# Optimization experiments

Hardware: AMD Instinct MI355X
Metric: run time of the kernel (lower is better)

Reference implementation:

```python
import math
import jax
import jax.numpy as jnp
import numpy as np

H = 16
D_MODEL = 1024
D_K = D_MODEL // H            # 64
POS_DK = D_MODEL // 4 // H    # 16
EMB_DIM = D_MODEL // 4        # 256
MAX_DIST = 1000
RES = 20                      # RealEmbedding discretization resolution (3rd ctor arg)
N_EMB = 2 * MAX_DIST * RES + 1
B, NQ, NK = 2, 512, 512


def setup_inputs() -> dict:
    key0 = jax.random.key(0)
    ks = jax.random.split(key0, 16)
    s = 0.02

    def lin(k, din, dout):
        return (jax.random.normal(k, (din, dout), jnp.float32) * s,
                jnp.zeros((dout,), jnp.float32))

    Wq, bq = lin(ks[7], D_MODEL, D_MODEL)
    Wk, bk = lin(ks[8], D_MODEL, D_MODEL)
    Wv, bv = lin(ks[9], D_MODEL, D_MODEL)
    Wo, bo = lin(ks[10], D_MODEL, D_MODEL)
    Wb, bb = lin(ks[11], POS_DK, 1)
    return {
        "query": jax.random.normal(ks[0], (B, NQ, D_MODEL), jnp.float32),
        "key": jax.random.normal(ks[1], (B, NK, D_MODEL), jnp.float32),
        "value": jax.random.normal(ks[2], (B, NK, D_MODEL), jnp.float32),
        "query_x": jax.random.uniform(ks[3], (B, NQ), jnp.float32, 0.0, float(MAX_DIST)),
        "query_y": jax.random.uniform(ks[4], (B, NQ), jnp.float32, 0.0, float(MAX_DIST)),
        "key_x": jax.random.uniform(ks[5], (B, NK), jnp.float32, 0.0, float(MAX_DIST)),
        "key_y": jax.random.uniform(ks[6], (B, NK), jnp.float32, 0.0, float(MAX_DIST)),
        "Wq": Wq, "bq": bq, "Wk": Wk, "bk": bk, "Wv": Wv, "bv": bv,
        "Wo": Wo, "bo": bo,
        "x_table": jax.random.normal(ks[12], (N_EMB, EMB_DIM), jnp.float32) * s,
        "y_table": jax.random.normal(ks[13], (N_EMB, EMB_DIM), jnp.float32) * s,
        "Wb": Wb, "bb": bb,
    }


def _real_emb(table, d):
    # RealEmbedding: clamp real-valued distance to [-MAX_DIST, MAX_DIST],
    # discretize at resolution RES, nearest-neighbor table lookup.
    idx = jnp.round((jnp.clip(d, -MAX_DIST, MAX_DIST) + MAX_DIST) * RES).astype(jnp.int32)
    return table[idx]


def _forward(query, key, value, query_x, query_y, key_x, key_y,
             Wq, bq, Wk, bk, Wv, bv, Wo, bo, x_table, y_table, Wb, bb):
    b, nq, _ = query.shape
    nk = key.shape[1]
    # relative-position differences, layout (b, nk, nq) exactly as the torch expand
    x_diff = query_x[:, None, :] - key_x[:, :, None]
    y_diff = query_y[:, None, :] - key_y[:, :, None]
    pos_emb = _real_emb(x_table, x_diff) + _real_emb(y_table, y_diff)  # (b, nk, nq, EMB_DIM)
    pos_emb = pos_emb.reshape(b, nk, nq, H, POS_DK)
    att_bias = jax.nn.sigmoid((pos_emb @ Wb + bb)[..., 0])  # (b, nk, nq, H)
    # permute(0,3,1,2): (b, H, nk, nq); added to (b, H, nq, nk) scores (self-attn, nq==nk)
    att_bias = att_bias.transpose(0, 3, 1, 2)
    q = (query @ Wq + bq).reshape(b, nq, H, D_K).transpose(0, 2, 1, 3)
    k = (key @ Wk + bk).reshape(b, nk, H, D_K).transpose(0, 2, 1, 3)
    v = (value @ Wv + bv).reshape(b, nk, H, D_K).transpose(0, 2, 1, 3)
    scores = jnp.einsum('bhqd,bhkd->bhqk', q, k) / math.sqrt(D_K) + att_bias
    p_attn = jax.nn.softmax(scores, axis=-1)  # dropout p=0 / eval mode
    out = jnp.einsum('bhqk,bhkd->bhqd', p_attn, v)
    out = out.transpose(0, 2, 1, 3).reshape(b, nq, D_MODEL)
    return out @ Wo + bo


def reference(query, key, value, query_x, query_y, key_x, key_y,
              Wq, bq, Wk, bk, Wv, bv, Wo, bo, x_table, y_table, Wb, bb):
    return _forward(query, key, value, query_x, query_y, key_x, key_y,
                    Wq, bq, Wk, bk, Wv, bv, Wo, bo, x_table, y_table, Wb, bb)
```

## Files before the change

### kernel.cpp

```cpp
#include <hip/hip_runtime.h>
#include <math.h>

#define HH 16
#define DM 1024
#define DK 64
#define NE 40001
#define NB 2
#define NQS 512
#define NKS 512

typedef unsigned short ushort_t;
typedef __attribute__((ext_vector_type(8))) short short8v;
typedef __attribute__((ext_vector_type(4))) float f32x4;

__device__ __forceinline__ ushort_t f2bf(float f) {
    union { float f; unsigned u; } v; v.f = f;
    unsigned r = v.u + 0x7FFFu + ((v.u >> 16) & 1u);
    return (ushort_t)(r >> 16);
}
__device__ __forceinline__ unsigned pack2(float a, float b) {
    return (unsigned)f2bf(a) | ((unsigned)f2bf(b) << 16);
}
__device__ __forceinline__ float asf(unsigned u) {
    union { unsigned u; float f; } v; v.u = u; return v.f;
}

#define PROJ_F4   (NE * 64)
#define PROJ_TOT  (2 * PROJ_F4)
#define PREP_PROJ_BLKS 1024
#define PREP_WT_BLKS   512
#define PREP_QKV_BLKS  256

__global__ __launch_bounds__(256) void prep_k(
    const float* __restrict__ xt, const float* __restrict__ yt,
    const float* __restrict__ Wb,
    const float* __restrict__ wq, const float* __restrict__ wk,
    const float* __restrict__ wv, const float* __restrict__ wo,
    const float* __restrict__ xq, const float* __restrict__ xk, const float* __restrict__ xv,
    ushort_t* __restrict__ xproj, ushort_t* __restrict__ yproj,
    ushort_t* __restrict__ wqt, ushort_t* __restrict__ wkt,
    ushort_t* __restrict__ wvt, ushort_t* __restrict__ wot,
    ushort_t* __restrict__ qc, ushort_t* __restrict__ kc, ushort_t* __restrict__ vc)
{
    __shared__ float ls[64][68];
    const int bid = blockIdx.x;
    const int tid = threadIdx.x;

    if (bid < PREP_PROJ_BLKS) {
        const int c = tid & 3;
        const float4 wq4 = ((const float4*)Wb)[c];
#pragma unroll 4
        for (int f4 = bid * 256 + tid; f4 < PROJ_TOT; f4 += PREP_PROJ_BLKS * 256) {
            const int tsel = (f4 >= PROJ_F4);
            const int g = tsel ? f4 - PROJ_F4 : f4;
            const float* tab = tsel ? yt : xt;
            float4 v = ((const float4*)tab)[g];
            float p = v.x * wq4.x + v.y * wq4.y + v.z * wq4.z + v.w * wq4.w;
            p += __shfl_xor(p, 1);
            p += __shfl_xor(p, 2);
            if (c == 0) {
                ushort_t* dst = tsel ? yproj : xproj;
                const int i = g >> 6, h = (g >> 2) & 15;
                dst[i * 16 + h] = f2bf(p);
            }
        }
    } else if (bid < PREP_PROJ_BLKS + PREP_WT_BLKS) {
        const int b0 = bid - PREP_PROJ_BLKS;
#pragma unroll
        for (int it = 0; it < 2; ++it) {
            const int t = b0 + it * PREP_WT_BLKS;
            const int z = t >> 8;
            const int rem = t & 255;
            const int k0 = (rem >> 4) * 64, n0 = (rem & 15) * 64;
            const float* w = (z == 0) ? wq : ((z == 1) ? wk : ((z == 2) ? wv : wo));
            ushort_t* wt = (z == 0) ? wqt : ((z == 1) ? wkt : ((z == 2) ? wvt : wot));

            if (it) __syncthreads();
#pragma unroll
            for (int j = 0; j < 4; ++j) {
                int r = (tid >> 4) + j * 16;
                int c2 = (tid & 15) * 4;
                float4 v = *(const float4*)(w + (k0 + r) * 1024 + n0 + c2);
                *(float4*)&ls[r][c2] = v;
            }
            __syncthreads();

            const int n = tid >> 2, kq = (tid & 3) * 16;
            float e[16];
#pragma unroll
            for (int j = 0; j < 16; ++j) e[j] = ls[kq + j][n];
            uint4 o0, o1;
            o0.x = pack2(e[0], e[1]);   o0.y = pack2(e[2], e[3]);
            o0.z = pack2(e[4], e[5]);   o0.w = pack2(e[6], e[7]);
            o1.x = pack2(e[8], e[9]);   o1.y = pack2(e[10], e[11]);
            o1.z = pack2(e[12], e[13]); o1.w = pack2(e[14], e[15]);
            ushort_t* dp = wt + (n0 + n) * 1024 + k0 + kq;
            *(uint4*)(dp)     = o0;
            *(uint4*)(dp + 8) = o1;
        }
    } else {
        const int b0 = bid - (PREP_PROJ_BLKS + PREP_WT_BLKS);
#pragma unroll 4
        for (int f4 = b0 * 256 + tid; f4 < 786432; f4 += PREP_QKV_BLKS * 256) {
            const int z = f4 >> 18;
            const int g = f4 & 262143;
            const float* src = (z == 0) ? xq : ((z == 1) ? xk : xv);
            ushort_t* dst = (z == 0) ? qc : ((z == 1) ? kc : vc);
            float4 a = ((const float4*)src)[g];
            uint2 o;
            o.x = pack2(a.x, a.y); o.y = pack2(a.z, a.w);
            *reinterpret_cast<uint2*>(dst + g * 4) = o;
        }
    }
}

__global__ __launch_bounds__(256, 6) void biasqkv_k(
    const ushort_t* __restrict__ A0, const ushort_t* __restrict__ A1, const ushort_t* __restrict__ A2,
    const ushort_t* __restrict__ B0, const ushort_t* __restrict__ B1, const ushort_t* __restrict__ B2,
    const float* __restrict__ bi0, const float* __restrict__ bi1, const float* __restrict__ bi2,
    ushort_t* __restrict__ Yh0, ushort_t* __restrict__ Yh1, ushort_t* __restrict__ Yh2,
    const ushort_t* __restrict__ xproj, const ushort_t* __restrict__ yproj,
    const float* __restrict__ qx, const float* __restrict__ qy,
    const float* __restrict__ kx, const float* __restrict__ ky,
    const float* __restrict__ bbp,
    ushort_t* __restrict__ biasf)
{
    __shared__ ushort_t As[64][72];
    __shared__ ushort_t Bs[64][72];
    const int bid = blockIdx.x;
    const int tid = threadIdx.x;

    if (bid < 768) {
        const int z = bid >> 8, by = (bid >> 4) & 15, bx = bid & 15;
        const ushort_t* Ah = (z == 0) ? A0 : ((z == 1) ? A1 : A2);
        const ushort_t* Bp = (z == 0) ? B0 : ((z == 1) ? B1 : B2);
        const float* bi = (z == 0) ? bi0 : ((z == 1) ? bi1 : bi2);
        ushort_t* Yh = (z == 0) ? Yh0 : ((z == 1) ? Yh1 : Yh2);
        const int m0 = by * 64, n0 = bx * 64;
        const int lane = tid & 63, w = tid >> 6;
        const int wm = w >> 1, wn = w & 1;
        const int srow = tid >> 2, scg = (tid & 3) * 16;

        f32x4 acc[2][2] = {};
        uint4 arh0, arh1, brh0, brh1;

        auto loadA = [&](int kk) {
            const ushort_t* ap = Ah + (m0 + srow) * 1024 + kk + scg;
            arh0 = *(const uint4*)(ap);
            arh1 = *(const uint4*)(ap + 8);
        };
        auto loadB = [&](int kk) {
            const ushort_t* bp = Bp + (n0 + srow) * 1024 + kk + scg;
            brh0 = *(const uint4*)(bp);
            brh1 = *(const uint4*)(bp + 8);
        };
        loadA(0); loadB(0);

        const int fr = lane & 15;
        const int ko = (lane >> 4) * 8;

        for (int k0 = 0; k0 < 1024; k0 += 64) {
            __syncthreads();
            *(uint4*)&As[srow][scg]     = arh0;
            *(uint4*)&As[srow][scg + 8] = arh1;
            *(uint4*)&Bs[srow][scg]     = brh0;
            *(uint4*)&Bs[srow][scg + 8] = brh1;
            __syncthreads();
            if (k0 + 64 < 1024) { loadA(k0 + 64); loadB(k0 + 64); }
#pragma unroll
            for (int ks = 0; ks < 64; ks += 32) {
                short8v af0 = *(const short8v*)&As[wm * 32 + fr][ks + ko];
                short8v af1 = *(const short8v*)&As[wm * 32 + 16 + fr][ks + ko];
                short8v bf0 = *(const short8v*)&Bs[wn * 32 + fr][ks + ko];
                short8v bf1 = *(const short8v*)&Bs[wn * 32 + 16 + fr][ks + ko];
                acc[0][0] = __builtin_amdgcn_mfma_f32_16x16x32_bf16(af0, bf0, acc[0][0], 0, 0, 0);
                acc[0][1] = __builtin_amdgcn_mfma_f32_16x16x32_bf16(af0, bf1, acc[0][1], 0, 0, 0);
                acc[1][0] = __builtin_amdgcn_mfma_f32_16x16x32_bf16(af1, bf0, acc[1][0], 0, 0, 0);
                acc[1][1] = __builtin_amdgcn_mfma_f32_16x16x32_bf16(af1, bf1, acc[1][1], 0, 0, 0);
            }
        }

        const int cr = (lane >> 4) * 4;
        const int cc = lane & 15;
#pragma unroll
        for (int m = 0; m < 2; ++m) {
#pragma unroll
            for (int n = 0; n < 2; ++n) {
                int grow = m0 + wm * 32 + m * 16 + cr;
                int gcol = n0 + wn * 32 + n * 16 + cc;
                float bv = bi[gcol];
                int hh = gcol >> 6, dd = gcol & 63;
                if (z == 0) {
#pragma unroll
                    for (int j = 0; j < 4; ++j) {
                        int r = grow + j, bb_ = r >> 9, nn = r & 511;
                        Yh[((bb_ * HH + hh) * NQS + nn) * DK + dd] = f2bf(acc[m][n][j] + bv);
                    }
                } else if (z == 1) {
#pragma unroll
                    for (int j = 0; j < 4; ++j) {
                        int r = grow + j, bb_ = r >> 9, nn = r & 511;
                        Yh[((bb_ * HH + hh) * NQS + nn) * DK + dd] = f2bf((acc[m][n][j] + bv) * 0.125f);
                    }
                } else {
#pragma unroll
                    for (int j = 0; j < 4; ++j) {
                        int r = grow + j, bb_ = r >> 9, nn = r & 511;
                        Yh[((bb_ * HH + hh) * DK + dd) * NKS + nn] = f2bf(acc[m][n][j] + bv);
                    }
                }
            }
        }
    } else {
        const int r = bid - 768;
        const int b = r >> 10;
        const int kt = (r >> 5) & 31, qt = r & 31;
        const int ql = tid & 15, kl = tid >> 4;
        const int qg = qt * 16 + ql, kg = kt * 16 + kl;

        float dx = qx[b * NKS + kg] - kx[b * NQS + qg];
        float dy = qy[b * NKS + kg] - ky[b * NQS + qg];
        int ix = (int)rintf((fminf(fmaxf(dx, -1000.f), 1000.f) + 1000.f) * 20.f);
        int iy = (int)rintf((fminf(fmaxf(dy, -1000.f), 1000.f) + 1000.f) * 20.f);
        const float bb = bbp[0];

        uint4 xw0 = *(const uint4*)(xproj + ix * 16);
        uint4 xw1 = *(const uint4*)(xproj + ix * 16 + 8);
        uint4 yw0 = *(const uint4*)(yproj + iy * 16);
        uint4 yw1 = *(const uint4*)(yproj + iy * 16 + 8);

        float xa[16], ya[16];
        {
            unsigned u[8] = {xw0.x, xw0.y, xw0.z, xw0.w, xw1.x, xw1.y, xw1.z, xw1.w};
            unsigned v[8] = {yw0.x, yw0.y, yw0.z, yw0.w, yw1.x, yw1.y, yw1.z, yw1.w};
#pragma unroll
            for (int wv = 0; wv < 8; ++wv) {
                xa[2 * wv]     = asf(u[wv] << 16);
                xa[2 * wv + 1] = asf(u[wv] & 0xFFFF0000u);
                ya[2 * wv]     = asf(v[wv] << 16);
                ya[2 * wv + 1] = asf(v[wv] & 0xFFFF0000u);
            }
        }
        const int lane_j = ((kl >> 2) * 16 + ql) * 4 + (kl & 3);
#pragma unroll
        for (int h = 0; h < HH; ++h) {
            float t2 = xa[h] + ya[h] + bb;
            float sig = 1.f / (1.f + __expf(-t2));
            biasf[((b * HH + h) * 32 + kt) * (32 * 256) + qt * 256 + lane_j] = f2bf(sig);
        }
    }
}

__global__ __launch_bounds__(256, 4) void attn_k(
    const ushort_t* __restrict__ qbh, const ushort_t* __restrict__ kbh,
    const ushort_t* __restrict__ vtb, const ushort_t* __restrict__ biasf,
    ushort_t* __restrict__ attb)
{
    __shared__ ushort_t pst[4][16][40];
    __shared__ float obuf[4][16][76];
    __shared__ float mt[4][16], lt[4][16];

    const int tid = threadIdx.x;
    const int wid = tid >> 6, lane = tid & 63;
    const int q = lane & 15, g = lane >> 4;
    const int qt = blockIdx.x;
    const int h = blockIdx.y, b = blockIdx.z;
    const int bh = b * HH + h;

    const ushort_t* Qp = qbh + (bh * NQS + qt * 16 + q) * DK + g * 8;
    short8v qf0 = *(const short8v*)Qp;
    short8v qf1 = *(const short8v*)(Qp + 32);

    f32x4 oacc[4] = {};
    float m = -1e30f, l = 0.f;

#pragma unroll 2
    for (int c = 0; c < 4; ++c) {
        const int kc = wid * 128 + c * 32;
        const ushort_t* Kp = kbh + (bh * NKS + kc + q) * DK + g * 8;
        short8v kf00 = *(const short8v*)(Kp);
        short8v kf01 = *(const short8v*)(Kp + 32);
        short8v kf10 = *(const short8v*)(Kp + 16 * DK);
        short8v kf11 = *(const short8v*)(Kp + 16 * DK + 32);

        f32x4 s0 = {0.f, 0.f, 0.f, 0.f};
        f32x4 s1 = {0.f, 0.f, 0.f, 0.f};
        s0 = __builtin_amdgcn_mfma_f32_16x16x32_bf16(kf00, qf0, s0, 0, 0, 0);
        s0 = __builtin_amdgcn_mfma_f32_16x16x32_bf16(kf01, qf1, s0, 0, 0, 0);
        s1 = __builtin_amdgcn_mfma_f32_16x16x32_bf16(kf10, qf0, s1, 0, 0, 0);
        s1 = __builtin_amdgcn_mfma_f32_16x16x32_bf16(kf11, qf1, s1, 0, 0, 0);

        const int kt = kc >> 4;
        uint2 b0 = *((const uint2*)(biasf + ((bh * 32 + kt) * 32 + qt) * 256) + lane);
        uint2 b1 = *((const uint2*)(biasf + ((bh * 32 + kt + 1) * 32 + qt) * 256) + lane);

        float sv[8];
        sv[0] = s0[0] + asf(b0.x << 16);
        sv[1] = s0[1] + asf(b0.x & 0xFFFF0000u);
        sv[2] = s0[2] + asf(b0.y << 16);
        sv[3] = s0[3] + asf(b0.y & 0xFFFF0000u);
        sv[4] = s1[0] + asf(b1.x << 16);
        sv[5] = s1[1] + asf(b1.x & 0xFFFF0000u);
        sv[6] = s1[2] + asf(b1.y << 16);
        sv[7] = s1[3] + asf(b1.y & 0xFFFF0000u);

        float mc = fmaxf(fmaxf(fmaxf(sv[0], sv[1]), fmaxf(sv[2], sv[3])),
                         fmaxf(fmaxf(sv[4], sv[5]), fmaxf(sv[6], sv[7])));
        mc = fmaxf(mc, __shfl_xor(mc, 16));
        mc = fmaxf(mc, __shfl_xor(mc, 32));
        float mn = fmaxf(m, mc);

        float p[8], ps = 0.f;
#pragma unroll
        for (int j = 0; j < 8; ++j) { p[j] = __expf(sv[j] - mn); ps += p[j]; }
        float sc = __expf(m - mn);
        l = l * sc + ps;
        m = mn;
#pragma unroll
        for (int dt = 0; dt < 4; ++dt)
#pragma unroll
            for (int j = 0; j < 4; ++j) oacc[dt][j] *= sc;

        ushort_t* prow = &pst[wid][q][0];
        *(unsigned*)(prow + 4 * g)          = pack2(p[0], p[1]);
        *(unsigned*)(prow + 4 * g + 2)      = pack2(p[2], p[3]);
        *(unsigned*)(prow + 16 + 4 * g)     = pack2(p[4], p[5]);
        *(unsigned*)(prow + 16 + 4 * g + 2) = pack2(p[6], p[7]);
        short8v pf = *(const short8v*)&pst[wid][q][8 * g];

        const ushort_t* Vp = vtb + (bh * DK + q) * NKS + kc + g * 8;
#pragma unroll
        for (int dt = 0; dt < 4; ++dt) {
            short8v vf = *(const short8v*)(Vp + dt * 16 * NKS);
            oacc[dt] = __builtin_amdgcn_mfma_f32_16x16x32_bf16(vf, pf, oacc[dt], 0, 0, 0);
        }
    }

    float lr = l + __shfl_xor(l, 16);
    lr = lr + __shfl_xor(lr, 32);
    if (lane < 16) { mt[wid][lane] = m; lt[wid][lane] = lr; }
#pragma unroll
    for (int dt = 0; dt < 4; ++dt)
#pragma unroll
        for (int j = 0; j < 4; ++j)
            obuf[wid][q][dt * 16 + 4 * g + j] = oacc[dt][j];
    __syncthreads();

    const int mq = tid >> 4, d4 = (tid & 15) * 4;
    float m0 = mt[0][mq], m1 = mt[1][mq], m2 = mt[2][mq], m3 = mt[3][mq];
    float ms = fmaxf(fmaxf(m0, m1), fmaxf(m2, m3));
    float e0 = __expf(m0 - ms), e1 = __expf(m1 - ms);
    float e2 = __expf(m2 - ms), e3 = __expf(m3 - ms);
    float denom = lt[0][mq] * e0 + lt[1][mq] * e1 + lt[2][mq] * e2 + lt[3][mq] * e3;
    float inv = 1.f / denom;
    float4 o0 = *(float4*)&obuf[0][mq][d4];
    float4 o1 = *(float4*)&obuf[1][mq][d4];
    float4 o2 = *(float4*)&obuf[2][mq][d4];
    float4 o3 = *(float4*)&obuf[3][mq][d4];
    float r0 = (o0.x * e0 + o1.x * e1 + o2.x * e2 + o3.x * e3) * inv;
    float r1 = (o0.y * e0 + o1.y * e1 + o2.y * e2 + o3.y * e3) * inv;
    float r2 = (o0.z * e0 + o1.z * e1 + o2.z * e2 + o3.z * e3) * inv;
    float r3 = (o0.w * e0 + o1.w * e1 + o2.w * e2 + o3.w * e3) * inv;
    uint2 ow;
    ow.x = pack2(r0, r1); ow.y = pack2(r2, r3);
    *reinterpret_cast<uint2*>(attb + (b * NQS + qt * 16 + mq) * DM + h * DK + d4) = ow;
}

__global__ __launch_bounds__(256) void ogemm_k(
    const ushort_t* __restrict__ Ah, const ushort_t* __restrict__ Bp,
    const float* __restrict__ bi, float* __restrict__ Yf)
{
    __shared__ ushort_t As[64][72];
    __shared__ ushort_t Bs[64][72];
    const int m0 = blockIdx.y * 64, n0 = blockIdx.x * 64;
    const int tid = threadIdx.x;
    const int lane = tid & 63, w = tid >> 6;
    const int wm = w >> 1, wn = w & 1;
    const int srow = tid >> 2, scg = (tid & 3) * 16;

    f32x4 acc[2][2] = {};
    uint4 arh0, arh1, brh0, brh1;

    auto loadA = [&](int kk) {
        const ushort_t* ap = Ah + (m0 + srow) * 1024 + kk + scg;
        arh0 = *(const uint4*)(ap);
        arh1 = *(const uint4*)(ap + 8);
    };
    auto loadB = [&](int kk) {
        const ushort_t* bp = Bp + (n0 + srow) * 1024 + kk + scg;
        brh0 = *(const uint4*)(bp);
        brh1 = *(const uint4*)(bp + 8);
    };
    loadA(0); loadB(0);

    const int fr = lane & 15;
    const int ko = (lane >> 4) * 8;

    for (int k0 = 0; k0 < 1024; k0 += 64) {
        __syncthreads();
        *(uint4*)&As[srow][scg]     = arh0;
        *(uint4*)&As[srow][scg + 8] = arh1;
        *(uint4*)&Bs[srow][scg]     = brh0;
        *(uint4*)&Bs[srow][scg + 8] = brh1;
        __syncthreads();
        if (k0 + 64 < 1024) { loadA(k0 + 64); loadB(k0 + 64); }
#pragma unroll
        for (int ks = 0; ks < 64; ks += 32) {
            short8v af0 = *(const short8v*)&As[wm * 32 + fr][ks + ko];
            short8v af1 = *(const short8v*)&As[wm * 32 + 16 + fr][ks + ko];
            short8v bf0 = *(const short8v*)&Bs[wn * 32 + fr][ks + ko];
            short8v bf1 = *(const short8v*)&Bs[wn * 32 + 16 + fr][ks + ko];
            acc[0][0] = __builtin_amdgcn_mfma_f32_16x16x32_bf16(af0, bf0, acc[0][0], 0, 0, 0);
            acc[0][1] = __builtin_amdgcn_mfma_f32_16x16x32_bf16(af0, bf1, acc[0][1], 0, 0, 0);
            acc[1][0] = __builtin_amdgcn_mfma_f32_16x16x32_bf16(af1, bf0, acc[1][0], 0, 0, 0);
            acc[1][1] = __builtin_amdgcn_mfma_f32_16x16x32_bf16(af1, bf1, acc[1][1], 0, 0, 0);
        }
    }

    const int cr = (lane >> 4) * 4;
    const int cc = lane & 15;
#pragma unroll
    for (int m = 0; m < 2; ++m) {
#pragma unroll
        for (int n = 0; n < 2; ++n) {
            int grow = m0 + wm * 32 + m * 16 + cr;
            int gcol = n0 + wn * 32 + n * 16 + cc;
            float bv = bi[gcol];
#pragma unroll
            for (int j = 0; j < 4; ++j)
                Yf[(grow + j) * 1024 + gcol] = acc[m][n][j] + bv;
        }
    }
}

extern "C" void kernel_launch(void* const* d_in, const int* in_sizes, int n_in,
                              void* d_out, int out_size, void* d_ws, size_t ws_size,
                              hipStream_t stream)
{
    const float* query = (const float*)d_in[0];
    const float* key   = (const float*)d_in[1];
    const float* value = (const float*)d_in[2];
    const float* qx    = (const float*)d_in[3];
    const float* qy    = (const float*)d_in[4];
    const float* kx    = (const float*)d_in[5];
    const float* ky    = (const float*)d_in[6];
    const float* Wq    = (const float*)d_in[7];
    const float* bq    = (const float*)d_in[8];
    const float* Wk    = (const float*)d_in[9];
    const float* bk    = (const float*)d_in[10];
    const float* Wv    = (const float*)d_in[11];
    const float* bv    = (const float*)d_in[12];
    const float* Wo    = (const float*)d_in[13];
    const float* bo    = (const float*)d_in[14];
    const float* xt    = (const float*)d_in[15];
    const float* yt    = (const float*)d_in[16];
    const float* Wb    = (const float*)d_in[17];
    const float* bbp   = (const float*)d_in[18];
    float* out = (float*)d_out;

    ushort_t* xprojh = (ushort_t*)d_ws;
    ushort_t* yprojh = xprojh + 640064;
    ushort_t* biasf  = yprojh + 640064;
    ushort_t* qbh    = biasf + 8388608;
    ushort_t* kbh    = qbh + 1048576;
    ushort_t* vtb    = kbh + 1048576;
    ushort_t* attb   = vtb + 1048576;
    ushort_t* wqt    = attb + 1048576;
    ushort_t* wkt    = wqt + 1048576;
    ushort_t* wvt    = wkt + 1048576;
    ushort_t* wot    = wvt + 1048576;
    ushort_t* qc     = wot + 1048576;
    ushort_t* kc     = qc + 1048576;
    ushort_t* vc     = kc + 1048576;

    prep_k<<<dim3(PREP_PROJ_BLKS + PREP_WT_BLKS + PREP_QKV_BLKS), dim3(256), 0, stream>>>(
        xt, yt, Wb, Wq, Wk, Wv, Wo, query, key, value,
        xprojh, yprojh, wqt, wkt, wvt, wot, qc, kc, vc);
    biasqkv_k<<<dim3(768 + 2048), dim3(256), 0, stream>>>(
        qc, kc, vc, wqt, wkt, wvt, bq, bk, bv, qbh, kbh, vtb,
        xprojh, yprojh, qx, qy, kx, ky, bbp, biasf);
    attn_k<<<dim3(32, 16, 2), dim3(256), 0, stream>>>(
        qbh, kbh, vtb, biasf, attb);
    ogemm_k<<<dim3(16, 16), dim3(256), 0, stream>>>(
        attb, wot, bo, out);
}
```

Before: 78.33 us.

## Fuse fp32-to-bf16 conversion into QKV GEMM and overlap with table projection

The separate prep pass that converted query/key/value and Wq/Wk/Wv to bf16 (and transposed the weights) is removed. The QKV projection GEMM now reads fp32 activations and weights directly, converting and transposing in registers before writing to shared memory. That GEMM is interleaved in one launch with the table-projection and Wo-transpose blocks, so the work that reads the embedding tables overlaps with the matrix multiply. The bias computation becomes its own kernel. This cuts a global round trip of bf16 intermediates, but the GEMM now issues fp32 loads and scattered 2-byte shared-memory stores for B, which may cause bank conflicts and extra per-iteration conversion work.

```diff
diff --git a/kernel.cpp b/kernel.cpp
--- a/kernel.cpp
+++ b/kernel.cpp
@@ -27,30 +27,33 @@
 
 #define PROJ_F4   (NE * 64)
 #define PROJ_TOT  (2 * PROJ_F4)
-#define PREP_PROJ_BLKS 1024
-#define PREP_WT_BLKS   512
-#define PREP_QKV_BLKS  256
-
-__global__ __launch_bounds__(256) void prep_k(
+#define K1_BLKS   2048
+
+__global__ __launch_bounds__(256, 4) void fused1_k(
     const float* __restrict__ xt, const float* __restrict__ yt,
     const float* __restrict__ Wb,
     const float* __restrict__ wq, const float* __restrict__ wk,
     const float* __restrict__ wv, const float* __restrict__ wo,
-    const float* __restrict__ xq, const float* __restrict__ xk, const float* __restrict__ xv,
+    const float* __restrict__ query, const float* __restrict__ key, const float* __restrict__ value,
+    const float* __restrict__ bq, const float* __restrict__ bk, const float* __restrict__ bv,
     ushort_t* __restrict__ xproj, ushort_t* __restrict__ yproj,
-    ushort_t* __restrict__ wqt, ushort_t* __restrict__ wkt,
-    ushort_t* __restrict__ wvt, ushort_t* __restrict__ wot,
-    ushort_t* __restrict__ qc, ushort_t* __restrict__ kc, ushort_t* __restrict__ vc)
+    ushort_t* __restrict__ wot,
+    ushort_t* __restrict__ qbh, ushort_t* __restrict__ kbh, ushort_t* __restrict__ vtb)
 {
-    __shared__ float ls[64][68];
+    __shared__ __align__(16) unsigned char smem[18944];
+    ushort_t (*As)[72] = (ushort_t(*)[72])smem;
+    ushort_t (*Bs)[72] = (ushort_t(*)[72])(smem + 9472);
+    float (*ls)[68] = (float(*)[68])smem;
+
     const int bid = blockIdx.x;
     const int tid = threadIdx.x;
 
-    if (bid < PREP_PROJ_BLKS) {
+    if (!(bid & 1)) {
+        const int pb = bid >> 1;
         const int c = tid & 3;
         const float4 wq4 = ((const float4*)Wb)[c];
 #pragma unroll 4
-        for (int f4 = bid * 256 + tid; f4 < PROJ_TOT; f4 += PREP_PROJ_BLKS * 256) {
+        for (int f4 = pb * 256 + tid; f4 < PROJ_TOT; f4 += 1024 * 256) {
             const int tsel = (f4 >= PROJ_F4);
             const int g = tsel ? f4 - PROJ_F4 : f4;
             const float* tab = tsel ? yt : xt;
@@ -64,190 +67,181 @@
                 dst[i * 16 + h] = f2bf(p);
             }
         }
-    } else if (bid < PREP_PROJ_BLKS + PREP_WT_BLKS) {
-        const int b0 = bid - PREP_PROJ_BLKS;
-#pragma unroll
-        for (int it = 0; it < 2; ++it) {
-            const int t = b0 + it * PREP_WT_BLKS;
-            const int z = t >> 8;
-            const int rem = t & 255;
-            const int k0 = (rem >> 4) * 64, n0 = (rem & 15) * 64;
-            const float* w = (z == 0) ? wq : ((z == 1) ? wk : ((z == 2) ? wv : wo));
-            ushort_t* wt = (z == 0) ? wqt : ((z == 1) ? wkt : ((z == 2) ? wvt : wot));
-
-            if (it) __syncthreads();
-#pragma unroll
-            for (int j = 0; j < 4; ++j) {
-                int r = (tid >> 4) + j * 16;
-                int c2 = (tid & 15) * 4;
-                float4 v = *(const float4*)(w + (k0 + r) * 1024 + n0 + c2);
-                *(float4*)&ls[r][c2] = v;
+        return;
+    }
+
+    const int u = bid >> 1;
+    if (u >= 768) {
+        const int rem = u - 768;
+        const int k0 = (rem >> 4) * 64, n0 = (rem & 15) * 64;
+#pragma unroll
+        for (int j = 0; j < 4; ++j) {
+            int r = (tid >> 4) + j * 16;
+            int c2 = (tid & 15) * 4;
+            float4 v = *(const float4*)(wo + (k0 + r) * 1024 + n0 + c2);
+            *(float4*)&ls[r][c2] = v;
+        }
+        __syncthreads();
+        const int n = tid >> 2, kq = (tid & 3) * 16;
+        float e[16];
+#pragma unroll
+        for (int j = 0; j < 16; ++j) e[j] = ls[kq + j][n];
+        uint4 o0, o1;
+        o0.x = pack2(e[0], e[1]);   o0.y = pack2(e[2], e[3]);
+        o0.z = pack2(e[4], e[5]);   o0.w = pack2(e[6], e[7]);
+        o1.x = pack2(e[8], e[9]);   o1.y = pack2(e[10], e[11]);
+        o1.z = pack2(e[12], e[13]); o1.w = pack2(e[14], e[15]);
+        ushort_t* dp = wot + (n0 + n) * 1024 + k0 + kq;
+        *(uint4*)(dp)     = o0;
+        *(uint4*)(dp + 8) = o1;
+        return;
+    }
+
+    const int z = u >> 8, by = (u >> 4) & 15, bx = u & 15;
+    const float* Af = (z == 0) ? query : ((z == 1) ? key : value);
+    const float* Wf = (z == 0) ? wq : ((z == 1) ? wk : wv);
+    const float* bi = (z == 0) ? bq : ((z == 1) ? bk : bv);
+    ushort_t* Yh = (z == 0) ? qbh : ((z == 1) ? kbh : vtb);
+    const int m0 = by * 64, n0 = bx * 64;
+    const int lane = tid & 63, w = tid >> 6;
+    const int wm = w >> 1, wn = w & 1;
+    const int srow = tid >> 2, scg = (tid & 3) * 16;
+    const int br_ = tid >> 4, bc = (tid & 15) * 4;
+
+    f32x4 acc[2][2] = {};
+    float4 arf0, arf1, arf2, arf3;
+    float4 brf0, brf1, brf2, brf3;
+
+    auto loadA = [&](int kk) {
+        const float* ap = Af + (m0 + srow) * 1024 + kk + scg;
+        arf0 = *(const float4*)(ap);
+        arf1 = *(const float4*)(ap + 4);
+        arf2 = *(const float4*)(ap + 8);
+        arf3 = *(const float4*)(ap + 12);
+    };
+    auto loadB = [&](int kk) {
+        brf0 = *(const float4*)(Wf + (kk + br_)      * 1024 + n0 + bc);
+        brf1 = *(const float4*)(Wf + (kk + br_ + 16) * 1024 + n0 + bc);
+        brf2 = *(const float4*)(Wf + (kk + br_ + 32) * 1024 + n0 + bc);
+        brf3 = *(const float4*)(Wf + (kk + br_ + 48) * 1024 + n0 + bc);
+    };
+    loadA(0); loadB(0);
+
+    const int fr = lane & 15;
+    const int ko = (lane >> 4) * 8;
+
+    for (int k0 = 0; k0 < 1024; k0 += 64) {
+        __syncthreads();
+        {
+            uint4 w0, w1;
+            w0.x = pack2(arf0.x, arf0.y); w0.y = pack2(arf0.z, arf0.w);
+            w0.z = pack2(arf1.x, arf1.y); w0.w = pack2(arf1.z, arf1.w);
+            w1.x = pack2(arf2.x, arf2.y); w1.y = pack2(arf2.z, arf2.w);
+            w1.z = pack2(arf3.x, arf3.y); w1.w = pack2(arf3.z, arf3.w);
+            *(uint4*)&As[srow][scg]     = w0;
+            *(uint4*)&As[srow][scg + 8] = w1;
+        }
+        {
+            Bs[bc + 0][br_] = f2bf(brf0.x); Bs[bc + 1][br_] = f2bf(brf0.y);
+            Bs[bc + 2][br_] = f2bf(brf0.z); Bs[bc + 3][br_] = f2bf(brf0.w);
+            Bs[bc + 0][br_ + 16] = f2bf(brf1.x); Bs[bc + 1][br_ + 16] = f2bf(brf1.y);
+            Bs[bc + 2][br_ + 16] = f2bf(brf1.z); Bs[bc + 3][br_ + 16] = f2bf(brf1.w);
+            Bs[bc + 0][br_ + 32] = f2bf(brf2.x); Bs[bc + 1][br_ + 32] = f2bf(brf2.y);
+            Bs[bc + 2][br_ + 32] = f2bf(brf2.z); Bs[bc + 3][br_ + 32] = f2bf(brf2.w);
+            Bs[bc + 0][br_ + 48] = f2bf(brf3.x); Bs[bc + 1][br_ + 48] = f2bf(brf3.y);
+            Bs[bc + 2][br_ + 48] = f2bf(brf3.z); Bs[bc + 3][br_ + 48] = f2bf(brf3.w);
+        }
+        __syncthreads();
+        if (k0 + 64 < 1024) { loadA(k0 + 64); loadB(k0 + 64); }
+#pragma unroll
+        for (int ks = 0; ks < 64; ks += 32) {
+            short8v af0 = *(const short8v*)&As[wm * 32 + fr][ks + ko];
+            short8v af1 = *(const short8v*)&As[wm * 32 + 16 + fr][ks + ko];
+            short8v bf0 = *(const short8v*)&Bs[wn * 32 + fr][ks + ko];
+            short8v bf1 = *(const short8v*)&Bs[wn * 32 + 16 + fr][ks + ko];
+            acc[0][0] = __builtin_amdgcn_mfma_f32_16x16x32_bf16(af0, bf0, acc[0][0], 0, 0, 0);
+            acc[0][1] = __builtin_amdgcn_mfma_f32_16x16x32_bf16(af0, bf1, acc[0][1], 0, 0, 0);
+            acc[1][0] = __builtin_amdgcn_mfma_f32_16x16x32_bf16(af1, bf0, acc[1][0], 0, 0, 0);
+            acc[1][1] = __builtin_amdgcn_mfma_f32_16x16x32_bf16(af1, bf1, acc[1][1], 0, 0, 0);
+        }
+    }
+
+    const int cr = (lane >> 4) * 4;
+    const int cc = lane & 15;
+#pragma unroll
+    for (int m = 0; m < 2; ++m) {
+#pragma unroll
+        for (int n = 0; n < 2; ++n) {
+            int grow = m0 + wm * 32 + m * 16 + cr;
+            int gcol = n0 + wn * 32 + n * 16 + cc;
+            float bv = bi[gcol];
+            int hh = gcol >> 6, dd = gcol & 63;
+            if (z == 0) {
+#pragma unroll
+                for (int j = 0; j < 4; ++j) {
+                    int r = grow + j, bb_ = r >> 9, nn = r & 511;
+                    Yh[((bb_ * HH + hh) * NQS + nn) * DK + dd] = f2bf(acc[m][n][j] + bv);
+                }
+            } else if (z == 1) {
+#pragma unroll
+                for (int j = 0; j < 4; ++j) {
+                    int r = grow + j, bb_ = r >> 9, nn = r & 511;
+                    Yh[((bb_ * HH + hh) * NQS + nn) * DK + dd] = f2bf((acc[m][n][j] + bv) * 0.125f);
+                }
+            } else {
+#pragma unroll
+                for (int j = 0; j < 4; ++j) {
+                    int r = grow + j, bb_ = r >> 9, nn = r & 511;
+                    Yh[((bb_ * HH + hh) * DK + dd) * NKS + nn] = f2bf(acc[m][n][j] + bv);
+                }
             }
-            __syncthreads();
-
-            const int n = tid >> 2, kq = (tid & 3) * 16;
-            float e[16];
-#pragma unroll
-            for (int j = 0; j < 16; ++j) e[j] = ls[kq + j][n];
-            uint4 o0, o1;
-            o0.x = pack2(e[0], e[1]);   o0.y = pack2(e[2], e[3]);
-            o0.z = pack2(e[4], e[5]);   o0.w = pack2(e[6], e[7]);
-            o1.x = pack2(e[8], e[9]);   o1.y = pack2(e[10], e[11]);
-            o1.z = pack2(e[12], e[13]); o1.w = pack2(e[14], e[15]);
-            ushort_t* dp = wt + (n0 + n) * 1024 + k0 + kq;
-            *(uint4*)(dp)     = o0;
-            *(uint4*)(dp + 8) = o1;
-        }
-    } else {
-        const int b0 = bid - (PREP_PROJ_BLKS + PREP_WT_BLKS);
-#pragma unroll 4
-        for (int f4 = b0 * 256 + tid; f4 < 786432; f4 += PREP_QKV_BLKS * 256) {
-            const int z = f4 >> 18;
-            const int g = f4 & 262143;
-            const float* src = (z == 0) ? xq : ((z == 1) ? xk : xv);
-            ushort_t* dst = (z == 0) ? qc : ((z == 1) ? kc : vc);
-            float4 a = ((const float4*)src)[g];
-            uint2 o;
-            o.x = pack2(a.x, a.y); o.y = pack2(a.z, a.w);
-            *reinterpret_cast<uint2*>(dst + g * 4) = o;
-        }
-    }
-}
-
-__global__ __launch_bounds__(256, 6) void biasqkv_k(
-    const ushort_t* __restrict__ A0, const ushort_t* __restrict__ A1, const ushort_t* __restrict__ A2,
-    const ushort_t* __restrict__ B0, const ushort_t* __restrict__ B1, const ushort_t* __restrict__ B2,
-    const float* __restrict__ bi0, const float* __restrict__ bi1, const float* __restrict__ bi2,
-    ushort_t* __restrict__ Yh0, ushort_t* __restrict__ Yh1, ushort_t* __restrict__ Yh2,
+        }
+    }
+}
+
+__global__ __launch_bounds__(256) void bias_k(
     const ushort_t* __restrict__ xproj, const ushort_t* __restrict__ yproj,
     const float* __restrict__ qx, const float* __restrict__ qy,
     const float* __restrict__ kx, const float* __restrict__ ky,
     const float* __restrict__ bbp,
     ushort_t* __restrict__ biasf)
 {
-    __shared__ ushort_t As[64][72];
-    __shared__ ushort_t Bs[64][72];
-    const int bid = blockIdx.x;
     const int tid = threadIdx.x;
-
-    if (bid < 768) {
-        const int z = bid >> 8, by = (bid >> 4) & 15, bx = bid & 15;
-        const ushort_t* Ah = (z == 0) ? A0 : ((z == 1) ? A1 : A2);
-        const ushort_t* Bp = (z == 0) ? B0 : ((z == 1) ? B1 : B2);
-        const float* bi = (z == 0) ? bi0 : ((z == 1) ? bi1 : bi2);
-        ushort_t* Yh = (z == 0) ? Yh0 : ((z == 1) ? Yh1 : Yh2);
-        const int m0 = by * 64, n0 = bx * 64;
-        const int lane = tid & 63, w = tid >> 6;
-        const int wm = w >> 1, wn = w & 1;
-        const int srow = tid >> 2, scg = (tid & 3) * 16;
-
-        f32x4 acc[2][2] = {};
-        uint4 arh0, arh1, brh0, brh1;
-
-        auto loadA = [&](int kk) {
-            const ushort_t* ap = Ah + (m0 + srow) * 1024 + kk + scg;
-            arh0 = *(const uint4*)(ap);
-            arh1 = *(const uint4*)(ap + 8);
-        };
-        auto loadB = [&](int kk) {
-            const ushort_t* bp = Bp + (n0 + srow) * 1024 + kk + scg;
-            brh0 = *(const uint4*)(bp);
-            brh1 = *(const uint4*)(bp + 8);
-        };
-        loadA(0); loadB(0);
-
-        const int fr = lane & 15;
-        const int ko = (lane >> 4) * 8;
-
-        for (int k0 = 0; k0 < 1024; k0 += 64) {
-            __syncthreads();
-            *(uint4*)&As[srow][scg]     = arh0;
-            *(uint4*)&As[srow][scg + 8] = arh1;
-            *(uint4*)&Bs[srow][scg]     = brh0;
-            *(uint4*)&Bs[srow][scg + 8] = brh1;
-            __syncthreads();
-            if (k0 + 64 < 1024) { loadA(k0 + 64); loadB(k0 + 64); }
-#pragma unroll
-            for (int ks = 0; ks < 64; ks += 32) {
-                short8v af0 = *(const short8v*)&As[wm * 32 + fr][ks + ko];
-                short8v af1 = *(const short8v*)&As[wm * 32 + 16 + fr][ks + ko];
-                short8v bf0 = *(const short8v*)&Bs[wn * 32 + fr][ks + ko];
-                short8v bf1 = *(const short8v*)&Bs[wn * 32 + 16 + fr][ks + ko];
-                acc[0][0] = __builtin_amdgcn_mfma_f32_16x16x32_bf16(af0, bf0, acc[0][0], 0, 0, 0);
-                acc[0][1] = __builtin_amdgcn_mfma_f32_16x16x32_bf16(af0, bf1, acc[0][1], 0, 0, 0);
-                acc[1][0] = __builtin_amdgcn_mfma_f32_16x16x32_bf16(af1, bf0, acc[1][0], 0, 0, 0);
-                acc[1][1] = __builtin_amdgcn_mfma_f32_16x16x32_bf16(af1, bf1, acc[1][1], 0, 0, 0);
-            }
-        }
-
-        const int cr = (lane >> 4) * 4;
-        const int cc = lane & 15;
-#pragma unroll
-        for (int m = 0; m < 2; ++m) {
-#pragma unroll
-            for (int n = 0; n < 2; ++n) {
-                int grow = m0 + wm * 32 + m * 16 + cr;
-                int gcol = n0 + wn * 32 + n * 16 + cc;
-                float bv = bi[gcol];
-                int hh = gcol >> 6, dd = gcol & 63;
-                if (z == 0) {
-#pragma unroll
-                    for (int j = 0; j < 4; ++j) {
-                        int r = grow + j, bb_ = r >> 9, nn = r & 511;
-                        Yh[((bb_ * HH + hh) * NQS + nn) * DK + dd] = f2bf(acc[m][n][j] + bv);
-                    }
-                } else if (z == 1) {
-#pragma unroll
-                    for (int j = 0; j < 4; ++j) {
-                        int r = grow + j, bb_ = r >> 9, nn = r & 511;
-                        Yh[((bb_ * HH + hh) * NQS + nn) * DK + dd] = f2bf((acc[m][n][j] + bv) * 0.125f);
-                    }
-                } else {
-#pragma unroll
-                    for (int j = 0; j < 4; ++j) {
-                        int r = grow + j, bb_ = r >> 9, nn = r & 511;
-                        Yh[((bb_ * HH + hh) * DK + dd) * NKS + nn] = f2bf(acc[m][n][j] + bv);
-                    }
-                }
-            }
-        }
-    } else {
-        const int r = bid - 768;
-        const int b = r >> 10;
-        const int kt = (r >> 5) & 31, qt = r & 31;
-        const int ql = tid & 15, kl = tid >> 4;
-        const int qg = qt * 16 + ql, kg = kt * 16 + kl;
-
-        float dx = qx[b * NKS + kg] - kx[b * NQS + qg];
-        float dy = qy[b * NKS + kg] - ky[b * NQS + qg];
-        int ix = (int)rintf((fminf(fmaxf(dx, -1000.f), 1000.f) + 1000.f) * 20.f);
-        int iy = (int)rintf((fminf(fmaxf(dy, -1000.f), 1000.f) + 1000.f) * 20.f);
-        const float bb = bbp[0];
-
-        uint4 xw0 = *(const uint4*)(xproj + ix * 16);
-        uint4 xw1 = *(const uint4*)(xproj + ix * 16 + 8);
-        uint4 yw0 = *(const uint4*)(yproj + iy * 16);
-        uint4 yw1 = *(const uint4*)(yproj + iy * 16 + 8);
-
-        float xa[16], ya[16];
-        {
-            unsigned u[8] = {xw0.x, xw0.y, xw0.z, xw0.w, xw1.x, xw1.y, xw1.z, xw1.w};
-            unsigned v[8] = {yw0.x, yw0.y, yw0.z, yw0.w, yw1.x, yw1.y, yw1.z, yw1.w};
-#pragma unroll
-            for (int wv = 0; wv < 8; ++wv) {
-                xa[2 * wv]     = asf(u[wv] << 16);
-                xa[2 * wv + 1] = asf(u[wv] & 0xFFFF0000u);
-                ya[2 * wv]     = asf(v[wv] << 16);
-                ya[2 * wv + 1] = asf(v[wv] & 0xFFFF0000u);
-            }
-        }
-        const int lane_j = ((kl >> 2) * 16 + ql) * 4 + (kl & 3);
-#pragma unroll
-        for (int h = 0; h < HH; ++h) {
-            float t2 = xa[h] + ya[h] + bb;
-            float sig = 1.f / (1.f + __expf(-t2));
-            biasf[((b * HH + h) * 32 + kt) * (32 * 256) + qt * 256 + lane_j] = f2bf(sig);
-        }
+    const int r = blockIdx.x;
+    const int b = r >> 10;
+    const int kt = (r >> 5) & 31, qt = r & 31;
+    const int ql = tid & 15, kl = tid >> 4;
+    const int qg = qt * 16 + ql, kg = kt * 16 + kl;
+
+    float dx = qx[b * NKS + kg] - kx[b * NQS + qg];
+    float dy = qy[b * NKS + kg] - ky[b * NQS + qg];
+    int ix = (int)rintf((fminf(fmaxf(dx, -1000.f), 1000.f) + 1000.f) * 20.f);
+    int iy = (int)rintf((fminf(fmaxf(dy, -1000.f), 1000.f) + 1000.f) * 20.f);
+    const float bb = bbp[0];
+
+    uint4 xw0 = *(const uint4*)(xproj + ix * 16);
+    uint4 xw1 = *(const uint4*)(xproj + ix * 16 + 8);
+    uint4 yw0 = *(const uint4*)(yproj + iy * 16);
+    uint4 yw1 = *(const uint4*)(yproj + iy * 16 + 8);
+
+    float xa[16], ya[16];
+    {
+        unsigned uu[8] = {xw0.x, xw0.y, xw0.z, xw0.w, xw1.x, xw1.y, xw1.z, xw1.w};
+        unsigned vv[8] = {yw0.x, yw0.y, yw0.z, yw0.w, yw1.x, yw1.y, yw1.z, yw1.w};
+#pragma unroll
+        for (int wv = 0; wv < 8; ++wv) {
+            xa[2 * wv]     = asf(uu[wv] << 16);
+            xa[2 * wv + 1] = asf(uu[wv] & 0xFFFF0000u);
+            ya[2 * wv]     = asf(vv[wv] << 16);
+            ya[2 * wv + 1] = asf(vv[wv] & 0xFFFF0000u);
+        }
+    }
+    const int lane_j = ((kl >> 2) * 16 + ql) * 4 + (kl & 3);
+#pragma unroll
+    for (int h = 0; h < HH; ++h) {
+        float t2 = xa[h] + ya[h] + bb;
+        float sig = 1.f / (1.f + __expf(-t2));
+        biasf[((b * HH + h) * 32 + kt) * (32 * 256) + qt * 256 + lane_j] = f2bf(sig);
     }
 }
 
@@ -465,19 +459,12 @@
     ushort_t* kbh    = qbh + 1048576;
     ushort_t* vtb    = kbh + 1048576;
     ushort_t* attb   = vtb + 1048576;
-    ushort_t* wqt    = attb + 1048576;
-    ushort_t* wkt    = wqt + 1048576;
-    ushort_t* wvt    = wkt + 1048576;
-    ushort_t* wot    = wvt + 1048576;
-    ushort_t* qc     = wot + 1048576;
-    ushort_t* kc     = qc + 1048576;
-    ushort_t* vc     = kc + 1048576;
-
-    prep_k<<<dim3(PREP_PROJ_BLKS + PREP_WT_BLKS + PREP_QKV_BLKS), dim3(256), 0, stream>>>(
-        xt, yt, Wb, Wq, Wk, Wv, Wo, query, key, value,
-        xprojh, yprojh, wqt, wkt, wvt, wot, qc, kc, vc);
-    biasqkv_k<<<dim3(768 + 2048), dim3(256), 0, stream>>>(
-        qc, kc, vc, wqt, wkt, wvt, bq, bk, bv, qbh, kbh, vtb,
+    ushort_t* wot    = attb + 1048576;
+
+    fused1_k<<<dim3(K1_BLKS), dim3(256), 0, stream>>>(
+        xt, yt, Wb, Wq, Wk, Wv, Wo, query, key, value, bq, bk, bv,
+        xprojh, yprojh, wot, qbh, kbh, vtb);
+    bias_k<<<dim3(2048), dim3(256), 0, stream>>>(
         xprojh, yprojh, qx, qy, kx, ky, bbp, biasf);
     attn_k<<<dim3(32, 16, 2), dim3(256), 0, stream>>>(
         qbh, kbh, vtb, biasf, attb);
```

New measurement: 113.4 us. 44.8% more time.
